# Optimization experiments

Hardware: AMD Instinct MI355X
Metric: run time of the kernel (lower is better)

## Reference

```python
import jax, jax.numpy as jnp
import numpy as np

EMBED = 1024
HEADS = 16
HEAD_DIM = EMBED // HEADS

def setup_inputs() -> dict:
    key = jax.random.key(0)
    ks = jax.random.split(key, 12)
    N, L, E = 4, 2048, EMBED
    s = 1.0 / np.sqrt(E)
    return {
        "values": jax.random.normal(ks[0], (N, L, E), jnp.float32),
        "keys": jax.random.normal(ks[1], (N, L, E), jnp.float32),
        "query": jax.random.normal(ks[2], (N, L, E), jnp.float32),
        "mask": jnp.ones((N, 1, 1, L), jnp.int32),
        "Wv": jax.random.normal(ks[3], (E, E), jnp.float32) * s,
        "bv": jnp.zeros((E,), jnp.float32),
        "Wk": jax.random.normal(ks[4], (E, E), jnp.float32) * s,
        "bk": jnp.zeros((E,), jnp.float32),
        "Wq": jax.random.normal(ks[5], (E, E), jnp.float32) * s,
        "bq": jnp.zeros((E,), jnp.float32),
        "Wo": jax.random.normal(ks[6], (E, E), jnp.float32) * s,
        "bo": jnp.zeros((E,), jnp.float32),
    }

def reference(values, keys, query, mask, Wv, bv, Wk, bk, Wq, bq, Wo, bo):
    N, L, E = values.shape
    H, D = HEADS, HEAD_DIM
    v = (values @ Wv + bv).reshape(N, L, H, D)
    k = (keys @ Wk + bk).reshape(N, L, H, D)
    q = (query @ Wq + bq).reshape(N, L, H, D)
    # energy: [N, H, Lq, Lk]
    energy = jnp.einsum('nqhd,nkhd->nhqk', q, k)
    energy = jnp.where(mask == 0, jnp.float32(-1e20), energy)
    attn = jax.nn.softmax(energy / np.sqrt(D), axis=3)
    out = jnp.einsum('nhqk,nkhd->nqhd', attn, v).reshape(N, L, E)
    return out @ Wo + bo
```

## Files before the change

### kernel.cpp

```cpp
#include <hip/hip_runtime.h>
#include <hip/hip_bf16.h>


#define N_B 4
#define L_S 2048
#define E_D 1024
#define H_N 16
#define D_H 64

typedef __attribute__((ext_vector_type(8))) short short8;
typedef __attribute__((ext_vector_type(8))) unsigned short ushort8;
typedef __attribute__((ext_vector_type(4))) unsigned short ushort4v;
typedef __attribute__((ext_vector_type(4))) float f32x4;
typedef __attribute__((ext_vector_type(16))) float f32x16;
typedef __attribute__((ext_vector_type(4))) unsigned int uint4v;

#define EXP2F(x) __builtin_amdgcn_exp2f(x)

__device__ __forceinline__ unsigned short f2b(float f) {
    unsigned int u = __builtin_bit_cast(unsigned int, f);
    u += 0x7fffu + ((u >> 16) & 1u);
    return (unsigned short)(u >> 16);
}

__device__ __forceinline__ void gload16(const void* g, void* l) {
    __builtin_amdgcn_global_load_lds(
        (const __attribute__((address_space(1))) void*)g,
        (__attribute__((address_space(3))) void*)l, 16, 0, 0);
}

__device__ __forceinline__ unsigned int cvtpk(float a, float b) {
    unsigned int w;
    asm("v_cvt_pk_bf16_f32 %0, %1, %2" : "=v"(w) : "v"(a), "v"(b));
    return w;
}

__global__ __launch_bounds__(256) void cvt3_kernel(const float* __restrict__ v,
                                                   const float* __restrict__ k,
                                                   const float* __restrict__ q,
                                                   unsigned short* __restrict__ out) {
    int z = blockIdx.y;
    const float* in = (z == 0) ? v : ((z == 1) ? k : q);
    unsigned short* o = out + (size_t)z * (8u << 20);
    size_t i = (size_t)blockIdx.x * 256 + threadIdx.x;
    const float* p = in + i * 8;
    ushort8 ov;
#pragma unroll
    for (int j = 0; j < 8; j++) ov[j] = f2b(p[j]);
    *(ushort8*)(o + i * 8) = ov;
}

__global__ __launch_bounds__(256) void wtrans4_kernel(const float* __restrict__ W0,
                                                      const float* __restrict__ W1,
                                                      const float* __restrict__ W2,
                                                      const float* __restrict__ W3,
                                                      unsigned short* __restrict__ WtBase) {
    __shared__ float t[64][65];
    int z = blockIdx.z;
    const float* W = (z == 0) ? W0 : ((z == 1) ? W1 : ((z == 2) ? W2 : W3));
    unsigned short* Wt = WtBase + (size_t)z * (1u << 20);
    int bx = blockIdx.x, by = blockIdx.y;
    int tx = threadIdx.x;
    int r0 = tx >> 4;
    int c4 = (tx & 15) << 2;
#pragma unroll
    for (int rr = 0; rr < 64; rr += 16) {
        const float* src = W + (size_t)(by * 64 + rr + r0) * E_D + bx * 64 + c4;
        float4 v = *(const float4*)src;
        t[rr + r0][c4 + 0] = v.x; t[rr + r0][c4 + 1] = v.y;
        t[rr + r0][c4 + 2] = v.z; t[rr + r0][c4 + 3] = v.w;
    }
    __syncthreads();
#pragma unroll
    for (int rr = 0; rr < 64; rr += 16) {
        int nrow = bx * 64 + rr + r0;
        ushort4v o;
#pragma unroll
        for (int j = 0; j < 4; j++) o[j] = f2b(t[c4 + j][rr + r0]);
        *(ushort4v*)(Wt + (size_t)nrow * E_D + by * 64 + c4) = o;
    }
}

template <int OUTMODE>
__device__ __forceinline__ void gemm_body(
    const unsigned short* __restrict__ A, const unsigned short* __restrict__ Bt,
    const float* __restrict__ bias, void* __restrict__ C,
    int K, int Nc, float scale,
    unsigned short* As, unsigned short* Bs, int n0, int m0) {
    int lane = threadIdx.x & 63, wave = threadIdx.x >> 6;
    int wr = (wave >> 1) * 64, wc = (wave & 1) * 64;
    f32x4 acc[4][4] = {};
    int nk = K >> 6;
    for (int kt = 0; kt < nk; ++kt) {
#pragma unroll
        for (int i = 0; i < 4; i++) {
            int c = (i * 4 + wave) * 64 + lane;
            int row = c >> 3;
            int csw = (c & 7) ^ (row & 7);
            gload16(A + (size_t)(m0 + row) * K + kt * 64 + csw * 8,
                    As + (size_t)(i * 4 + wave) * 512);
            gload16(Bt + (size_t)(n0 + row) * K + kt * 64 + csw * 8,
                    Bs + (size_t)(i * 4 + wave) * 512);
        }
        __syncthreads();
#pragma unroll
        for (int ks = 0; ks < 2; ++ks) {
            short8 a[4], b[4];
#pragma unroll
            for (int mi = 0; mi < 4; mi++) {
                int row = wr + mi * 16 + (lane & 15);
                int ch = (ks * 4 + (lane >> 4)) ^ (row & 7);
                a[mi] = *(const short8*)(As + row * 64 + ch * 8);
            }
#pragma unroll
            for (int ni = 0; ni < 4; ni++) {
                int col = wc + ni * 16 + (lane & 15);
                int ch = (ks * 4 + (lane >> 4)) ^ (col & 7);
                b[ni] = *(const short8*)(Bs + col * 64 + ch * 8);
            }
#pragma unroll
            for (int mi = 0; mi < 4; mi++)
#pragma unroll
                for (int ni = 0; ni < 4; ni++)
                    acc[mi][ni] = __builtin_amdgcn_mfma_f32_16x16x32_bf16(
                        a[mi], b[ni], acc[mi][ni], 0, 0, 0);
        }
        __syncthreads();
    }
    if (OUTMODE == 2) {
        int g = lane >> 4, c = lane & 15;
        unsigned short* tb = As + wave * 4096;
#pragma unroll
        for (int ni = 0; ni < 4; ni++) {
            int cl = ni * 16 + c;
            float bb = bias[n0 + wc + cl];
#pragma unroll
            for (int mi = 0; mi < 4; mi++) {
#pragma unroll
                for (int r = 0; r < 4; r++) {
                    int rl = mi * 16 + g * 4 + r;
                    tb[rl * 64 + (((cl >> 3) ^ (rl & 7)) << 3) + (cl & 7)] =
                        f2b((acc[mi][ni][r] + bb) * scale);
                }
            }
        }
        int mrow = m0 + wr;
        int n = mrow >> 11;
        int l0 = mrow & 2047;
        int h = (n0 + wc) >> 6;
        unsigned short* vt = (unsigned short*)C;
#pragma unroll
        for (int i = 0; i < 8; i++) {
            int d = i * 8 + (lane >> 3);
            int lc = (lane & 7) * 8;
            ushort8 ov;
#pragma unroll
            for (int j = 0; j < 8; j++) {
                int rl = lc + j;
                ov[j] = tb[rl * 64 + (((d >> 3) ^ (rl & 7)) << 3) + (d & 7)];
            }
            *(ushort8*)(vt + (size_t)((n * H_N + h) * D_H + d) * L_S + l0 + lc) = ov;
        }
        return;
    }
#pragma unroll
    for (int ni = 0; ni < 4; ni++) {
        int col = n0 + wc + ni * 16 + (lane & 15);
        float bb = bias[col];
#pragma unroll
        for (int mi = 0; mi < 4; mi++) {
            int rbase = m0 + wr + mi * 16 + (lane >> 4) * 4;
#pragma unroll
            for (int r = 0; r < 4; r++) {
                float v = (acc[mi][ni][r] + bb) * scale;
                if (OUTMODE == 1)
                    ((float*)C)[(size_t)(rbase + r) * Nc + col] = v;
                else
                    ((unsigned short*)C)[(size_t)(rbase + r) * Nc + col] = f2b(v);
            }
        }
    }
}

template <int OUTMODE>
__global__ __launch_bounds__(256, 2) void gemm_kernel(
    const unsigned short* __restrict__ A, const unsigned short* __restrict__ Bt,
    const float* __restrict__ bias, void* __restrict__ C,
    int M, int K, int Nc, float scale) {
    __shared__ unsigned short SMEM[2][128 * 64];
    gemm_body<OUTMODE>(A, Bt, bias, C, K, Nc, scale, SMEM[0], SMEM[1],
                       blockIdx.x * 128, blockIdx.y * 128);
}

__global__ __launch_bounds__(256, 2) void gemm3_kernel(
    const unsigned short* __restrict__ Abase, const unsigned short* __restrict__ Wtbase,
    const float* __restrict__ bv, const float* __restrict__ bk, const float* __restrict__ bq,
    unsigned short* __restrict__ vT, unsigned short* __restrict__ kbf,
    unsigned short* __restrict__ qbf, float qscale) {
    __shared__ unsigned short SMEM[2][128 * 64];
    int z = blockIdx.z;
    const unsigned short* A  = Abase + (size_t)z * (8u << 20);
    const unsigned short* Bt = Wtbase + (size_t)z * (1u << 20);
    int n0 = blockIdx.x * 128, m0 = blockIdx.y * 128;
    if (z == 0) {
        gemm_body<2>(A, Bt, bv, vT, E_D, E_D, 1.0f, SMEM[0], SMEM[1], n0, m0);
    } else if (z == 1) {
        gemm_body<0>(A, Bt, bk, kbf, E_D, E_D, 1.0f, SMEM[0], SMEM[1], n0, m0);
    } else {
        gemm_body<0>(A, Bt, bq, qbf, E_D, E_D, qscale, SMEM[0], SMEM[1], n0, m0);
    }
}

__global__ __launch_bounds__(512, 4) void attn_kernel(
    const unsigned short* __restrict__ qb, const unsigned short* __restrict__ kb,
    const unsigned short* __restrict__ vt, const int* __restrict__ mask,
    unsigned short* __restrict__ aout) {
    __shared__ unsigned short KV[4][64 * 64];
    __shared__ alignas(8) unsigned char okb[256];
    int lane = threadIdx.x & 63, wave = threadIdx.x >> 6;
    int qc = lane & 31, hl = lane >> 5;
    const float SHIFT = 20.0f;

    int bid = blockIdx.x;
    int xcd = bid & 7, idx = bid >> 3;
    int grp = xcd * 8 + (idx >> 3);
    int q0 = (idx & 7) * 256;
    int hd = grp & 15;
    int n = grp >> 4;

    const unsigned short* qptr  = qb + (size_t)n * L_S * E_D + hd * 64;
    const unsigned short* kbase = kb + (size_t)n * L_S * E_D + hd * 64;
    const unsigned short* vbase = vt + (size_t)(n * H_N + hd) * D_H * L_S;
    const int* mbase = mask + n * L_S;

    if (threadIdx.x < 256) {
        int t8 = threadIdx.x * 8;
        int4 ma = *(const int4*)(mbase + t8);
        int4 mb = *(const int4*)(mbase + t8 + 4);
        int ok = (ma.x != 0) & (ma.y != 0) & (ma.z != 0) & (ma.w != 0) &
                 (mb.x != 0) & (mb.y != 0) & (mb.z != 0) & (mb.w != 0);
        okb[threadIdx.x] = (unsigned char)ok;
    }
    unsigned short* Qs = &KV[0][0];
#pragma unroll
    for (int i = 0; i < 4; i++) {
        int ci = i * 8 + wave;
        int cc = ci * 64 + lane;
        int row = cc >> 3, csw = (cc & 7) ^ (row & 7);
        gload16(qptr + (size_t)(q0 + row) * E_D + csw * 8, Qs + (size_t)ci * 512);
    }
    __syncthreads();
    short8 qf[4];
#pragma unroll
    for (int dk = 0; dk < 4; dk++) {
        int row = wave * 32 + qc;
        int ch = (dk * 2 + hl) ^ (row & 7);
        qf[dk] = *(const short8*)(Qs + row * 64 + ch * 8);
    }
    asm volatile("s_waitcnt lgkmcnt(0)" ::: "memory");
    __syncthreads();
    {
        int cc = wave * 64 + lane;
        int row = cc >> 3, csw = (cc & 7) ^ (row & 7);
        gload16(kbase + (size_t)row * E_D + csw * 8, KV[0] + wave * 512);
        gload16(vbase + (size_t)row * L_S + csw * 8, KV[2] + wave * 512);
    }

    f32x16 o[2] = {};
    float lrun = 0.f;

    const int NT = L_S / 64;
    for (int kt = 0; kt < NT; ++kt) {
        int cur = kt & 1;
        if (kt + 1 < NT) {
            int cc = wave * 64 + lane;
            int row = cc >> 3, csw = (cc & 7) ^ (row & 7);
            gload16(kbase + (size_t)((kt + 1) * 64 + row) * E_D + csw * 8,
                    KV[cur ^ 1] + wave * 512);
            gload16(vbase + (size_t)row * L_S + (kt + 1) * 64 + csw * 8,
                    KV[2 + (cur ^ 1)] + wave * 512);
            asm volatile("s_waitcnt vmcnt(2)" ::: "memory");
        } else {
            asm volatile("s_waitcnt vmcnt(0)" ::: "memory");
        }
        __builtin_amdgcn_s_barrier();
        __builtin_amdgcn_sched_barrier(0);

        const unsigned short* KsC = KV[cur];
        const unsigned short* VsC = KV[2 + cur];

        f32x16 sT0 = {}, sT1 = {};
        __builtin_amdgcn_s_setprio(1);
#pragma unroll
        for (int dk = 0; dk < 4; dk++) {
            int kr0 = qc, kr1 = 32 + qc;
            int ch0 = (dk * 2 + hl) ^ (kr0 & 7);
            int ch1 = (dk * 2 + hl) ^ (kr1 & 7);
            short8 kf0 = *(const short8*)(KsC + kr0 * 64 + ch0 * 8);
            short8 kf1 = *(const short8*)(KsC + kr1 * 64 + ch1 * 8);
            sT0 = __builtin_amdgcn_mfma_f32_32x32x16_bf16(kf0, qf[dk], sT0, 0, 0, 0);
            sT1 = __builtin_amdgcn_mfma_f32_32x32x16_bf16(kf1, qf[dk], sT1, 0, 0, 0);
        }
        __builtin_amdgcn_s_setprio(0);

        uint2 fl = *(const uint2*)&okb[kt * 8];
        bool dense = ((fl.x & fl.y) == 0x01010101u);
        if (!dense) {
#pragma unroll
            for (int reg = 0; reg < 16; reg++) {
                int crow = (reg & 3) + 8 * (reg >> 2) + 4 * hl;
                int key = kt * 64 + crow;
                sT0[reg] += mbase[key] ? 0.f : -1e30f;
                sT1[reg] += mbase[key + 32] ? 0.f : -1e30f;
            }
        }
        float ps = 0.f;
#pragma unroll
        for (int kg = 0; kg < 2; kg++) {
            const f32x16& sS = (kg == 0) ? sT0 : sT1;
            float p[16];
#pragma unroll
            for (int r = 0; r < 16; r++) {
                p[r] = EXP2F(sS[r] - SHIFT);
                ps += p[r];
            }
            unsigned int w[8], ow[8];
#pragma unroll
            for (int a = 0; a < 8; a++) w[a] = cvtpk(p[2 * a], p[2 * a + 1]);
#pragma unroll
            for (int a = 0; a < 8; a++) ow[a] = __shfl_xor(w[a], 32);
            uint4v u0, u1;
            u0[0] = hl ? ow[2] : w[0];  u0[1] = hl ? ow[3] : w[1];
            u0[2] = hl ? w[2]  : ow[0]; u0[3] = hl ? w[3]  : ow[1];
            u1[0] = hl ? ow[6] : w[4];  u1[1] = hl ? ow[7] : w[5];
            u1[2] = hl ? w[6]  : ow[4]; u1[3] = hl ? w[7]  : ow[5];
            short8 pa0 = __builtin_bit_cast(short8, u0);
            short8 pa1 = __builtin_bit_cast(short8, u1);
            __builtin_amdgcn_s_setprio(1);
#pragma unroll
            for (int dg = 0; dg < 2; dg++) {
                int vr = dg * 32 + qc;
                int c0 = (kg * 4 + 0 + hl) ^ (vr & 7);
                int c1 = (kg * 4 + 2 + hl) ^ (vr & 7);
                short8 vb0 = *(const short8*)(VsC + vr * 64 + c0 * 8);
                short8 vb1 = *(const short8*)(VsC + vr * 64 + c1 * 8);
                o[dg] = __builtin_amdgcn_mfma_f32_32x32x16_bf16(pa0, vb0, o[dg], 0, 0, 0);
                o[dg] = __builtin_amdgcn_mfma_f32_32x32x16_bf16(pa1, vb1, o[dg], 0, 0, 0);
            }
            __builtin_amdgcn_s_setprio(0);
        }
        ps += __shfl_xor(ps, 32);
        lrun += ps;

        asm volatile("s_waitcnt lgkmcnt(0)" ::: "memory");
        __builtin_amdgcn_s_barrier();
    }
#pragma unroll
    for (int reg = 0; reg < 16; reg++) {
        int crow = (reg & 3) + 8 * (reg >> 2) + 4 * hl;
        float iv = 1.f / __shfl(lrun, crow);
        size_t rb = (size_t)(n * L_S + q0 + wave * 32 + crow) * E_D + hd * 64 + qc;
        aout[rb]      = f2b(o[0][reg] * iv);
        aout[rb + 32] = f2b(o[1][reg] * iv);
    }
}

extern "C" void kernel_launch(void* const* d_in, const int* in_sizes, int n_in,
                              void* d_out, int out_size, void* d_ws, size_t ws_size,
                              hipStream_t stream) {
    const float* values = (const float*)d_in[0];
    const float* keys   = (const float*)d_in[1];
    const float* query  = (const float*)d_in[2];
    const int*   mask   = (const int*)d_in[3];
    const float* Wv = (const float*)d_in[4];  const float* bv = (const float*)d_in[5];
    const float* Wk = (const float*)d_in[6];  const float* bk = (const float*)d_in[7];
    const float* Wq = (const float*)d_in[8];  const float* bq = (const float*)d_in[9];
    const float* Wo = (const float*)d_in[10]; const float* bo = (const float*)d_in[11];
    float* out = (float*)d_out;
    char* ws = (char*)d_ws;
    const size_t MB = 1ull << 20;
    unsigned short* xv  = (unsigned short*)(ws + 0 * MB);
    unsigned short* wtv = (unsigned short*)(ws + 48 * MB);
    unsigned short* wto = (unsigned short*)(ws + 54 * MB);
    unsigned short* vT  = (unsigned short*)(ws + 56 * MB);
    unsigned short* kbf = (unsigned short*)(ws + 72 * MB);
    unsigned short* qbf = (unsigned short*)(ws + 88 * MB);
    unsigned short* aob = (unsigned short*)(ws + 16 * MB);

    const float QS = 0.125f * 1.4426950408889634f;

    cvt3_kernel<<<dim3(4096, 3), 256, 0, stream>>>(values, keys, query, xv);
    wtrans4_kernel<<<dim3(16, 16, 4), 256, 0, stream>>>(Wv, Wk, Wq, Wo, wtv);
    gemm3_kernel<<<dim3(E_D / 128, (N_B * L_S) / 128, 3), 256, 0, stream>>>(
        xv, wtv, bv, bk, bq, vT, kbf, qbf, QS);
    attn_kernel<<<dim3(512), 512, 0, stream>>>(qbf, kbf, vT, mask, aob);
    gemm_kernel<1><<<dim3(E_D / 128, (N_B * L_S) / 128), 256, 0, stream>>>(
        aob, wto, bo, out, N_B * L_S, E_D, E_D, 1.0f);
}
```

Measured before the change: 214.3 us.

## Use chunk-major LDS layout for Q/K/V and permlane32_swap for P exchange

The shared-memory tiles for Q, K and V move from a row-major XOR-swizzled layout to a chunk-major layout, where each 8-element column chunk of all 64 rows is stored contiguously. Each wave now loads one chunk column per tile, which removes the swizzle arithmetic and makes fragment reads contiguous across lanes. The eight shfl_xor exchanges plus selects used to build the P operand are replaced by four permlane32_swap instructions. In exchange, global loads become strided across rows (one 16-byte segment per row per lane), which may lower coalescing efficiency.

```diff
diff --git a/kernel.cpp b/kernel.cpp
--- a/kernel.cpp
+++ b/kernel.cpp
@@ -14,6 +14,7 @@
 typedef __attribute__((ext_vector_type(4))) float f32x4;
 typedef __attribute__((ext_vector_type(16))) float f32x16;
 typedef __attribute__((ext_vector_type(4))) unsigned int uint4v;
+typedef __attribute__((ext_vector_type(2))) unsigned int uint2v;
 
 #define EXP2F(x) __builtin_amdgcn_exp2f(x)
 
@@ -244,27 +245,18 @@
     unsigned short* Qs = &KV[0][0];
 #pragma unroll
     for (int i = 0; i < 4; i++) {
-        int ci = i * 8 + wave;
-        int cc = ci * 64 + lane;
-        int row = cc >> 3, csw = (cc & 7) ^ (row & 7);
-        gload16(qptr + (size_t)(q0 + row) * E_D + csw * 8, Qs + (size_t)ci * 512);
+        gload16(qptr + (size_t)(q0 + wave * 32 + (lane & 31)) * E_D + (2 * i + (lane >> 5)) * 8,
+                Qs + wave * 2048 + i * 512);
     }
     __syncthreads();
     short8 qf[4];
 #pragma unroll
-    for (int dk = 0; dk < 4; dk++) {
-        int row = wave * 32 + qc;
-        int ch = (dk * 2 + hl) ^ (row & 7);
-        qf[dk] = *(const short8*)(Qs + row * 64 + ch * 8);
-    }
+    for (int dk = 0; dk < 4; dk++)
+        qf[dk] = *(const short8*)(Qs + wave * 2048 + (dk * 2 + hl) * 256 + qc * 8);
     asm volatile("s_waitcnt lgkmcnt(0)" ::: "memory");
     __syncthreads();
-    {
-        int cc = wave * 64 + lane;
-        int row = cc >> 3, csw = (cc & 7) ^ (row & 7);
-        gload16(kbase + (size_t)row * E_D + csw * 8, KV[0] + wave * 512);
-        gload16(vbase + (size_t)row * L_S + csw * 8, KV[2] + wave * 512);
-    }
+    gload16(kbase + (size_t)lane * E_D + wave * 8, KV[0] + wave * 512);
+    gload16(vbase + (size_t)lane * L_S + wave * 8, KV[2] + wave * 512);
 
     f32x16 o[2] = {};
     float lrun = 0.f;
@@ -273,11 +265,9 @@
     for (int kt = 0; kt < NT; ++kt) {
         int cur = kt & 1;
         if (kt + 1 < NT) {
-            int cc = wave * 64 + lane;
-            int row = cc >> 3, csw = (cc & 7) ^ (row & 7);
-            gload16(kbase + (size_t)((kt + 1) * 64 + row) * E_D + csw * 8,
+            gload16(kbase + (size_t)((kt + 1) * 64 + lane) * E_D + wave * 8,
                     KV[cur ^ 1] + wave * 512);
-            gload16(vbase + (size_t)row * L_S + (kt + 1) * 64 + csw * 8,
+            gload16(vbase + (size_t)lane * L_S + (kt + 1) * 64 + wave * 8,
                     KV[2 + (cur ^ 1)] + wave * 512);
             asm volatile("s_waitcnt vmcnt(2)" ::: "memory");
         } else {
@@ -293,11 +283,9 @@
         __builtin_amdgcn_s_setprio(1);
 #pragma unroll
         for (int dk = 0; dk < 4; dk++) {
-            int kr0 = qc, kr1 = 32 + qc;
-            int ch0 = (dk * 2 + hl) ^ (kr0 & 7);
-            int ch1 = (dk * 2 + hl) ^ (kr1 & 7);
-            short8 kf0 = *(const short8*)(KsC + kr0 * 64 + ch0 * 8);
-            short8 kf1 = *(const short8*)(KsC + kr1 * 64 + ch1 * 8);
+            int ch = (dk * 2 + hl) * 512;
+            short8 kf0 = *(const short8*)(KsC + ch + qc * 8);
+            short8 kf1 = *(const short8*)(KsC + ch + (32 + qc) * 8);
             sT0 = __builtin_amdgcn_mfma_f32_32x32x16_bf16(kf0, qf[dk], sT0, 0, 0, 0);
             sT1 = __builtin_amdgcn_mfma_f32_32x32x16_bf16(kf1, qf[dk], sT1, 0, 0, 0);
         }
@@ -324,26 +312,24 @@
                 p[r] = EXP2F(sS[r] - SHIFT);
                 ps += p[r];
             }
-            unsigned int w[8], ow[8];
+            unsigned int w[8];
 #pragma unroll
             for (int a = 0; a < 8; a++) w[a] = cvtpk(p[2 * a], p[2 * a + 1]);
-#pragma unroll
-            for (int a = 0; a < 8; a++) ow[a] = __shfl_xor(w[a], 32);
+            uint2v r02 = __builtin_amdgcn_permlane32_swap(w[0], w[2], false, false);
+            uint2v r13 = __builtin_amdgcn_permlane32_swap(w[1], w[3], false, false);
+            uint2v r46 = __builtin_amdgcn_permlane32_swap(w[4], w[6], false, false);
+            uint2v r57 = __builtin_amdgcn_permlane32_swap(w[5], w[7], false, false);
             uint4v u0, u1;
-            u0[0] = hl ? ow[2] : w[0];  u0[1] = hl ? ow[3] : w[1];
-            u0[2] = hl ? w[2]  : ow[0]; u0[3] = hl ? w[3]  : ow[1];
-            u1[0] = hl ? ow[6] : w[4];  u1[1] = hl ? ow[7] : w[5];
-            u1[2] = hl ? w[6]  : ow[4]; u1[3] = hl ? w[7]  : ow[5];
+            u0[0] = r02.x; u0[1] = r13.x; u0[2] = r02.y; u0[3] = r13.y;
+            u1[0] = r46.x; u1[1] = r57.x; u1[2] = r46.y; u1[3] = r57.y;
             short8 pa0 = __builtin_bit_cast(short8, u0);
             short8 pa1 = __builtin_bit_cast(short8, u1);
             __builtin_amdgcn_s_setprio(1);
 #pragma unroll
             for (int dg = 0; dg < 2; dg++) {
                 int vr = dg * 32 + qc;
-                int c0 = (kg * 4 + 0 + hl) ^ (vr & 7);
-                int c1 = (kg * 4 + 2 + hl) ^ (vr & 7);
-                short8 vb0 = *(const short8*)(VsC + vr * 64 + c0 * 8);
-                short8 vb1 = *(const short8*)(VsC + vr * 64 + c1 * 8);
+                short8 vb0 = *(const short8*)(VsC + (kg * 4 + hl) * 512 + vr * 8);
+                short8 vb1 = *(const short8*)(VsC + (kg * 4 + 2 + hl) * 512 + vr * 8);
                 o[dg] = __builtin_amdgcn_mfma_f32_32x32x16_bf16(pa0, vb0, o[dg], 0, 0, 0);
                 o[dg] = __builtin_amdgcn_mfma_f32_32x32x16_bf16(pa1, vb1, o[dg], 0, 0, 0);
             }
```

Result: faster. 208.9 us (-2.5%).
